# Performance work log

Measured on AMD Instinct MI355X. Metric: run time of the kernel, lower is better.

Reference implementation:

```python
import jax, jax.numpy as jnp
import numpy as np

HEAD_NUM = 16


def setup_inputs() -> dict:
    key = jax.random.key(0)
    ks = jax.random.split(key, 7)
    B, S, D = 4, 2048, 1024
    scale = 1.0 / np.sqrt(D)
    return {
        "q": jax.random.normal(ks[0], (B, S, D), jnp.float32),
        "k": jax.random.normal(ks[1], (B, S, D), jnp.float32),
        "v": jax.random.normal(ks[2], (B, S, D), jnp.float32),
        "w_q": jax.random.normal(ks[3], (D, D), jnp.float32) * scale,
        "w_k": jax.random.normal(ks[4], (D, D), jnp.float32) * scale,
        "w_v": jax.random.normal(ks[5], (D, D), jnp.float32) * scale,
        "w_o": jax.random.normal(ks[6], (D, D), jnp.float32) * scale,
    }


def reference(q, k, v, w_q, w_k, w_v, w_o):
    B, Sq, _ = q.shape
    H = HEAD_NUM
    d_k = w_q.shape[1] // H  # per-head key dim

    def split_heads(x):
        b, s, _ = x.shape
        return x.reshape(b, s, H, -1).transpose(0, 2, 1, 3)  # [b,h,s,d]

    hq = split_heads(q @ w_q)
    hk = split_heads(k @ w_k)
    hv = split_heads(v @ w_v)

    scores = jnp.einsum("bhqd,bhkd->bhqk", hq, hk) / jnp.sqrt(
        jnp.asarray(d_k, dtype=hq.dtype)
    )
    attn = jax.nn.softmax(scores, axis=-1)
    out = jnp.einsum("bhqk,bhkd->bhqd", attn, hv)  # [b,h,q,d]
    out = out.transpose(0, 2, 1, 3).reshape(B, Sq, -1)  # concat heads
    return out @ w_o
```

## Files before the change

### kernel.cpp

```cpp
#include <hip/hip_runtime.h>

typedef unsigned short u16;
typedef short vshort8 __attribute__((ext_vector_type(8)));
typedef __bf16 vbf16x8 __attribute__((ext_vector_type(8)));
typedef float vf32x4 __attribute__((ext_vector_type(4)));
typedef float vf32x16 __attribute__((ext_vector_type(16)));

__device__ __forceinline__ u16 f2bf(float f) {
  unsigned u = __builtin_bit_cast(unsigned, f);
  u += 0x7FFFu + ((u >> 16) & 1u);
  return (u16)(u >> 16);
}

__device__ __forceinline__ unsigned cvtpk(float lo, float hi) {
  unsigned r;
  asm("v_cvt_pk_bf16_f32 %0, %1, %2" : "=v"(r) : "v"(lo), "v"(hi));
  return r;
}

__device__ __forceinline__ vf32x4 mfma_bf16(vshort8 a, vshort8 b, vf32x4 c) {
  return __builtin_amdgcn_mfma_f32_16x16x32_bf16(
      __builtin_bit_cast(vbf16x8, a), __builtin_bit_cast(vbf16x8, b), c, 0, 0, 0);
}

__device__ __forceinline__ vf32x16 mfma32(vshort8 a, vshort8 b, vf32x16 c) {
  return __builtin_amdgcn_mfma_f32_32x32x16_bf16(
      __builtin_bit_cast(vbf16x8, a), __builtin_bit_cast(vbf16x8, b), c, 0, 0, 0);
}

__device__ __forceinline__ void gload16(const void* g, void* l) {
  __builtin_amdgcn_global_load_lds(
      (const __attribute__((address_space(1))) void*)g,
      (__attribute__((address_space(3))) void*)l, 16, 0, 0);
}

__global__ __launch_bounds__(256) void cvtk(const float* __restrict__ in,
                                            u16* __restrict__ out, int n4) {
  int idx = blockIdx.x * 256 + threadIdx.x;
  int stride = gridDim.x * 256;
  for (int i = idx; i < n4; i += stride) {
    float4 v = ((const float4*)in)[i];
    unsigned lo = (unsigned)f2bf(v.x) | ((unsigned)f2bf(v.y) << 16);
    unsigned hi = (unsigned)f2bf(v.z) | ((unsigned)f2bf(v.w) << 16);
    uint2 o; o.x = lo; o.y = hi;
    *(uint2*)&out[(size_t)i * 4] = o;
  }
}

__global__ __launch_bounds__(256) void wtrans(const float* __restrict__ W,
                                              u16* __restrict__ Wt) {
  __shared__ u16 tile[64][72];
  int t = threadIdx.x;
  int n0 = blockIdx.x * 64, k0 = blockIdx.y * 64;
#pragma unroll
  for (int it = 0; it < 4; ++it) {
    int cid = it * 256 + t;
    int r = cid >> 4, c4 = cid & 15;
    float4 v = *(const float4*)&W[(k0 + r) * 1024 + n0 + c4 * 4];
    u16* d = &tile[r][c4 * 4];
    d[0] = f2bf(v.x); d[1] = f2bf(v.y); d[2] = f2bf(v.z); d[3] = f2bf(v.w);
  }
  __syncthreads();
#pragma unroll
  for (int it = 0; it < 4; ++it) {
    int cid = it * 256 + t;
    int rn = cid >> 4, c4 = cid & 15;
    unsigned lo = (unsigned)tile[c4 * 4 + 0][rn] | ((unsigned)tile[c4 * 4 + 1][rn] << 16);
    unsigned hi = (unsigned)tile[c4 * 4 + 2][rn] | ((unsigned)tile[c4 * 4 + 3][rn] << 16);
    uint2 o; o.x = lo; o.y = hi;
    *(uint2*)&Wt[(n0 + rn) * 1024 + k0 + c4 * 4] = o;
  }
}

__global__ __launch_bounds__(256) void vtrans(const u16* __restrict__ V,
                                              u16* __restrict__ Vt) {
  __shared__ u16 tile[64][72];
  int t = threadIdx.x;
  int s0 = blockIdx.x * 64;
  int bh = blockIdx.y, b = bh >> 4, h = bh & 15;
#pragma unroll
  for (int it = 0; it < 2; ++it) {
    int cid = it * 256 + t;
    int r = cid >> 3, c8 = cid & 7;
    vshort8 v = *(const vshort8*)&V[(size_t)(b * 2048 + s0 + r) * 1024 + h * 64 + c8 * 8];
    *(vshort8*)&tile[r][c8 * 8] = v;
  }
  __syncthreads();
#pragma unroll
  for (int it = 0; it < 2; ++it) {
    int cid = it * 256 + t;
    int rd = cid >> 3, c8 = cid & 7;
    unsigned w[4];
#pragma unroll
    for (int j = 0; j < 4; ++j) {
      unsigned lo = tile[c8 * 8 + 2 * j][rd];
      unsigned hi = tile[c8 * 8 + 2 * j + 1][rd];
      w[j] = lo | (hi << 16);
    }
    uint4 o; o.x = w[0]; o.y = w[1]; o.z = w[2]; o.w = w[3];
    *(uint4*)&Vt[(size_t)(bh * 64 + rd) * 2048 + s0 + c8 * 8] = o;
  }
}

template <int OUTF32>
__global__ __launch_bounds__(256) void gemm_nt(const u16* __restrict__ A,
                                               const u16* __restrict__ Bt,
                                               float* __restrict__ Cf,
                                               u16* __restrict__ Cb,
                                               int M, int N, int K, float oscale) {
  __shared__ __align__(16) u16 As[128 * 64];
  __shared__ __align__(16) u16 Bs[128 * 64];
  int t = threadIdx.x, lane = t & 63, wid = t >> 6;
  int g = lane >> 4, i16 = lane & 15;
  int n0 = blockIdx.x * 128, m0 = blockIdx.y * 128;
  int wm = wid >> 1, wn = wid & 1;

  vf32x4 acc[4][4];
#pragma unroll
  for (int a = 0; a < 4; ++a)
#pragma unroll
    for (int b = 0; b < 4; ++b) acc[a][b] = (vf32x4){0.f, 0.f, 0.f, 0.f};

  int ldsbase = (wid * 64) * 8;
  for (int kt = 0; kt < K / 64; ++kt) {
    if (kt) __syncthreads();
#pragma unroll
    for (int it = 0; it < 4; ++it) {
      int cid = it * 256 + t;
      int row = cid >> 3, c = cid & 7, sc = c ^ (row & 7);
      gload16(A + (size_t)(m0 + row) * K + kt * 64 + sc * 8, &As[it * 2048 + ldsbase]);
    }
#pragma unroll
    for (int it = 0; it < 4; ++it) {
      int cid = it * 256 + t;
      int row = cid >> 3, c = cid & 7, sc = c ^ (row & 7);
      gload16(Bt + (size_t)(n0 + row) * K + kt * 64 + sc * 8, &Bs[it * 2048 + ldsbase]);
    }
    __syncthreads();
#pragma unroll
    for (int kc = 0; kc < 2; ++kc) {
      vshort8 af[4], bf[4];
#pragma unroll
      for (int mf = 0; mf < 4; ++mf) {
        int row = wm * 64 + mf * 16 + i16;
        int ch = (kc * 4 + g) ^ (row & 7);
        af[mf] = *(const vshort8*)&As[row * 64 + ch * 8];
      }
#pragma unroll
      for (int nf = 0; nf < 4; ++nf) {
        int row = wn * 64 + nf * 16 + i16;
        int ch = (kc * 4 + g) ^ (row & 7);
        bf[nf] = *(const vshort8*)&Bs[row * 64 + ch * 8];
      }
#pragma unroll
      for (int mf = 0; mf < 4; ++mf)
#pragma unroll
        for (int nf = 0; nf < 4; ++nf)
          acc[mf][nf] = mfma_bf16(af[mf], bf[nf], acc[mf][nf]);
    }
  }
#pragma unroll
  for (int mf = 0; mf < 4; ++mf)
#pragma unroll
    for (int nf = 0; nf < 4; ++nf)
#pragma unroll
      for (int r = 0; r < 4; ++r) {
        int m = m0 + wm * 64 + mf * 16 + g * 4 + r;
        int n = n0 + wn * 64 + nf * 16 + i16;
        if (OUTF32)
          Cf[(size_t)m * N + n] = acc[mf][nf][r] * oscale;
        else
          Cb[(size_t)m * N + n] = f2bf(acc[mf][nf][r] * oscale);
      }
}

__global__ __launch_bounds__(512, 2) void attn_fwd2(const u16* __restrict__ Q,
                                                    const u16* __restrict__ K,
                                                    const u16* __restrict__ Vt,
                                                    u16* __restrict__ O) {
  int t = threadIdx.x, lane = t & 63, w = t >> 6;
  int l31 = lane & 31, hi = lane >> 5;
  int i = blockIdx.x;
  int qb = (i >> 3) & 3;
  int bh = (i & 7) + 8 * (i >> 5);
  int b = bh >> 4, h = bh & 15;

  const u16* Qbase = Q + (size_t)(b * 2048 + qb * 512 + w * 64) * 1024 + h * 64;
  const u16* Kbase = K + (size_t)(b * 2048) * 1024 + h * 64;
  const u16* Vbase = Vt + (size_t)(bh * 64) * 2048;

  vshort8 qf[2][4];
#pragma unroll
  for (int fq = 0; fq < 2; ++fq)
#pragma unroll
    for (int dc = 0; dc < 4; ++dc)
      qf[fq][dc] = *(const vshort8*)&Qbase[(size_t)(fq * 32 + l31) * 1024 + dc * 16 + hi * 8];

  vf32x16 oacc[2][2];
#pragma unroll
  for (int dm = 0; dm < 2; ++dm)
#pragma unroll
    for (int fq = 0; fq < 2; ++fq)
#pragma unroll
      for (int r = 0; r < 16; ++r) oacc[dm][fq][r] = 0.f;
  float mrun[2] = {-3.0e38f, -3.0e38f}, lrun[2] = {0.f, 0.f};

  for (int kt = 0; kt < 32; ++kt) {
    __syncthreads();
    vshort8 kf[2][4], vtf[2][4];
#pragma unroll
    for (int ks = 0; ks < 2; ++ks)
#pragma unroll
      for (int dc = 0; dc < 4; ++dc)
        kf[ks][dc] = *(const vshort8*)&Kbase[(size_t)(kt * 64 + ks * 32 + l31) * 1024 + dc * 16 + hi * 8];
#pragma unroll
    for (int dm = 0; dm < 2; ++dm)
#pragma unroll
      for (int s = 0; s < 4; ++s)
        vtf[dm][s] = *(const vshort8*)&Vbase[(size_t)(dm * 32 + l31) * 2048 + kt * 64 + s * 16 + hi * 8];

    vf32x16 sacc[2][2];
#pragma unroll
    for (int ks = 0; ks < 2; ++ks)
#pragma unroll
      for (int fq = 0; fq < 2; ++fq)
#pragma unroll
        for (int r = 0; r < 16; ++r) sacc[ks][fq][r] = 0.f;

    __builtin_amdgcn_s_setprio(1);
#pragma unroll
    for (int dc = 0; dc < 4; ++dc)
#pragma unroll
      for (int ks = 0; ks < 2; ++ks)
#pragma unroll
        for (int fq = 0; fq < 2; ++fq)
          sacc[ks][fq] = mfma32(kf[ks][dc], qf[fq][dc], sacc[ks][fq]);
    __builtin_amdgcn_s_setprio(0);

#pragma unroll
    for (int fq = 0; fq < 2; ++fq) {
      float pmax = sacc[0][fq][0];
#pragma unroll
      for (int ks = 0; ks < 2; ++ks)
#pragma unroll
        for (int r = 0; r < 16; ++r) pmax = fmaxf(pmax, sacc[ks][fq][r]);
      pmax = fmaxf(pmax, __shfl_xor(pmax, 32));
      float mold = mrun[fq];
      if (pmax > mold + 8.f) {
        float al = exp2f(mold - pmax);
        lrun[fq] *= al;
#pragma unroll
        for (int dm = 0; dm < 2; ++dm)
#pragma unroll
          for (int r = 0; r < 16; ++r) oacc[dm][fq][r] *= al;
        mrun[fq] = pmax;
      }
      float mm = mrun[fq];
      float ssum = 0.f;
#pragma unroll
      for (int ks = 0; ks < 2; ++ks)
#pragma unroll
        for (int r = 0; r < 16; ++r) {
          float p = exp2f(sacc[ks][fq][r] - mm);
          sacc[ks][fq][r] = p;
          ssum += p;
        }
      ssum += __shfl_xor(ssum, 32);
      lrun[fq] += ssum;
    }

#pragma unroll
    for (int s = 0; s < 4; ++s) {
      vshort8 pb[2];
#pragma unroll
      for (int fq = 0; fq < 2; ++fq) {
        const int ks = s >> 1, s1 = s & 1;
        float a0 = sacc[ks][fq][8 * s1 + 0], a1 = sacc[ks][fq][8 * s1 + 1];
        float a2 = sacc[ks][fq][8 * s1 + 2], a3 = sacc[ks][fq][8 * s1 + 3];
        float b0 = sacc[ks][fq][8 * s1 + 4], b1 = sacc[ks][fq][8 * s1 + 5];
        float b2 = sacc[ks][fq][8 * s1 + 6], b3 = sacc[ks][fq][8 * s1 + 7];
        unsigned wA0 = cvtpk(a0, a1), wA1 = cvtpk(a2, a3);
        unsigned wB0 = cvtpk(b0, b1), wB1 = cvtpk(b2, b3);
        unsigned sA0 = hi ? wB0 : wA0, sA1 = hi ? wB1 : wA1;
        unsigned sd0 = hi ? wA0 : wB0, sd1 = hi ? wA1 : wB1;
        unsigned rv0 = __shfl_xor((int)sd0, 32), rv1 = __shfl_xor((int)sd1, 32);
        uint4 wv;
        wv.x = hi ? rv0 : sA0; wv.y = hi ? rv1 : sA1;
        wv.z = hi ? sA0 : rv0; wv.w = hi ? sA1 : rv1;
        pb[fq] = __builtin_bit_cast(vshort8, wv);
      }
      __builtin_amdgcn_s_setprio(1);
#pragma unroll
      for (int dm = 0; dm < 2; ++dm)
#pragma unroll
        for (int fq = 0; fq < 2; ++fq)
          oacc[dm][fq] = mfma32(vtf[dm][s], pb[fq], oacc[dm][fq]);
      __builtin_amdgcn_s_setprio(0);
    }
  }

#pragma unroll
  for (int fq = 0; fq < 2; ++fq) {
    float inv = 1.f / lrun[fq];
    size_t qrow = (size_t)(b * 2048 + qb * 512 + w * 64 + fq * 32 + l31);
#pragma unroll
    for (int dm = 0; dm < 2; ++dm)
#pragma unroll
      for (int u = 0; u < 4; ++u) {
        unsigned w0 = cvtpk(oacc[dm][fq][4 * u + 0] * inv, oacc[dm][fq][4 * u + 1] * inv);
        unsigned w1 = cvtpk(oacc[dm][fq][4 * u + 2] * inv, oacc[dm][fq][4 * u + 3] * inv);
        uint2 o; o.x = w0; o.y = w1;
        *(uint2*)&O[qrow * 1024 + h * 64 + dm * 32 + 8 * u + 4 * hi] = o;
      }
  }
}

extern "C" void kernel_launch(void* const* d_in, const int* in_sizes, int n_in,
                              void* d_out, int out_size, void* d_ws, size_t ws_size,
                              hipStream_t stream) {
  const float* q  = (const float*)d_in[0];
  const float* k  = (const float*)d_in[1];
  const float* v  = (const float*)d_in[2];
  const float* wq = (const float*)d_in[3];
  const float* wk = (const float*)d_in[4];
  const float* wv = (const float*)d_in[5];
  const float* wo = (const float*)d_in[6];
  float* out = (float*)d_out;

  const int M = 8192, D = 1024;
  u16* Qb = (u16*)d_out;
  u16* Kb = Qb + (size_t)M * D;
  u16* xb  = (u16*)d_ws;
  u16* Vb  = xb + (size_t)M * D;
  u16* Vtg = Vb + (size_t)M * D;
  u16* wqt = Vtg + (size_t)M * D;
  u16* wkt = wqt + (size_t)D * D;
  u16* wvt = wkt + (size_t)D * D;
  u16* wot = wvt + (size_t)D * D;

  dim3 blk(256);
  dim3 gw(16, 16);
  wtrans<<<gw, blk, 0, stream>>>(wq, wqt);
  wtrans<<<gw, blk, 0, stream>>>(wk, wkt);
  wtrans<<<gw, blk, 0, stream>>>(wv, wvt);
  wtrans<<<gw, blk, 0, stream>>>(wo, wot);

  const float QSCALE = 0.125f * 1.44269504088896f;
  int n4 = M * D / 4;
  dim3 ggemm(8, 64);
  cvtk<<<2048, blk, 0, stream>>>(q, xb, n4);
  gemm_nt<0><<<ggemm, blk, 0, stream>>>(xb, wqt, nullptr, Qb, M, D, D, QSCALE);
  cvtk<<<2048, blk, 0, stream>>>(k, xb, n4);
  gemm_nt<0><<<ggemm, blk, 0, stream>>>(xb, wkt, nullptr, Kb, M, D, D, 1.0f);
  cvtk<<<2048, blk, 0, stream>>>(v, xb, n4);
  gemm_nt<0><<<ggemm, blk, 0, stream>>>(xb, wvt, nullptr, Vb, M, D, D, 1.0f);

  vtrans<<<dim3(32, 64), blk, 0, stream>>>(Vb, Vtg);
  attn_fwd2<<<dim3(256), dim3(512), 0, stream>>>(Qb, Kb, Vtg, xb );
  gemm_nt<1><<<ggemm, blk, 0, stream>>>(xb, wot, out, nullptr, M, D, D, 1.0f);
}
```

Measured before the change: 311.2 us.

## Split attention into smaller blocks and batch conversion and weight-transpose launches

The attention kernel is restructured so each wave handles one 32-row query fragment instead of two, with 256-thread blocks and a 1024-block grid in place of 256 blocks of 512 threads. This raises the number of blocks and lowers per-wave register use, at the cost of loading K/V fragments twice as often per query row. The four weight-transpose launches are merged into one launch using a z-dimension. The q and k fp32-to-bf16 conversions now run in a single launch, with converted k staged in the Vt buffer before it is needed, which cuts launch count.

Result: slower. 373.6 us (+20.1%).

```diff
diff --git a/kernel.cpp b/kernel.cpp
--- a/kernel.cpp
+++ b/kernel.cpp
@@ -34,8 +34,13 @@
       (__attribute__((address_space(3))) void*)l, 16, 0, 0);
 }
 
-__global__ __launch_bounds__(256) void cvtk(const float* __restrict__ in,
-                                            u16* __restrict__ out, int n4) {
+__global__ __launch_bounds__(256) void cvtk2(const float* __restrict__ a,
+                                             const float* __restrict__ b,
+                                             u16* __restrict__ oa,
+                                             u16* __restrict__ ob, int n4) {
+  const float* in = blockIdx.y ? b : a;
+  u16* out = blockIdx.y ? ob : oa;
+  if (in == nullptr) return;
   int idx = blockIdx.x * 256 + threadIdx.x;
   int stride = gridDim.x * 256;
   for (int i = idx; i < n4; i += stride) {
@@ -47,8 +52,15 @@
   }
 }
 
-__global__ __launch_bounds__(256) void wtrans(const float* __restrict__ W,
-                                              u16* __restrict__ Wt) {
+__global__ __launch_bounds__(256) void wtrans4(const float* __restrict__ w0,
+                                               const float* __restrict__ w1,
+                                               const float* __restrict__ w2,
+                                               const float* __restrict__ w3,
+                                               u16* __restrict__ o0, u16* __restrict__ o1,
+                                               u16* __restrict__ o2, u16* __restrict__ o3) {
+  int z = blockIdx.z;
+  const float* W = z == 0 ? w0 : z == 1 ? w1 : z == 2 ? w2 : w3;
+  u16* Wt = z == 0 ? o0 : z == 1 ? o1 : z == 2 ? o2 : o3;
   __shared__ u16 tile[64][72];
   int t = threadIdx.x;
   int n0 = blockIdx.x * 64, k0 = blockIdx.y * 64;
@@ -174,145 +186,133 @@
       }
 }
 
-__global__ __launch_bounds__(512, 2) void attn_fwd2(const u16* __restrict__ Q,
+__global__ __launch_bounds__(256, 4) void attn_fwd3(const u16* __restrict__ Q,
                                                     const u16* __restrict__ K,
                                                     const u16* __restrict__ Vt,
                                                     u16* __restrict__ O) {
   int t = threadIdx.x, lane = t & 63, w = t >> 6;
   int l31 = lane & 31, hi = lane >> 5;
   int i = blockIdx.x;
-  int qb = (i >> 3) & 3;
-  int bh = (i & 7) + 8 * (i >> 5);
+  int bh = (i & 7) + 8 * (i >> 7);
+  int qc = (i >> 3) & 15;
   int b = bh >> 4, h = bh & 15;
 
-  const u16* Qbase = Q + (size_t)(b * 2048 + qb * 512 + w * 64) * 1024 + h * 64;
+  const u16* Qbase = Q + (size_t)(b * 2048 + qc * 128 + w * 32) * 1024 + h * 64;
   const u16* Kbase = K + (size_t)(b * 2048) * 1024 + h * 64;
   const u16* Vbase = Vt + (size_t)(bh * 64) * 2048;
 
-  vshort8 qf[2][4];
-#pragma unroll
-  for (int fq = 0; fq < 2; ++fq)
-#pragma unroll
-    for (int dc = 0; dc < 4; ++dc)
-      qf[fq][dc] = *(const vshort8*)&Qbase[(size_t)(fq * 32 + l31) * 1024 + dc * 16 + hi * 8];
-
-  vf32x16 oacc[2][2];
+  vshort8 qf[4];
+#pragma unroll
+  for (int dc = 0; dc < 4; ++dc)
+    qf[dc] = *(const vshort8*)&Qbase[(size_t)l31 * 1024 + dc * 16 + hi * 8];
+
+  vf32x16 oacc[2];
 #pragma unroll
   for (int dm = 0; dm < 2; ++dm)
 #pragma unroll
-    for (int fq = 0; fq < 2; ++fq)
-#pragma unroll
-      for (int r = 0; r < 16; ++r) oacc[dm][fq][r] = 0.f;
-  float mrun[2] = {-3.0e38f, -3.0e38f}, lrun[2] = {0.f, 0.f};
+    for (int r = 0; r < 16; ++r) oacc[dm][r] = 0.f;
+  float mrun = -3.0e38f, lrun = 0.f;
 
   for (int kt = 0; kt < 32; ++kt) {
     __syncthreads();
-    vshort8 kf[2][4], vtf[2][4];
+    vshort8 kf[2][4];
 #pragma unroll
     for (int ks = 0; ks < 2; ++ks)
 #pragma unroll
       for (int dc = 0; dc < 4; ++dc)
         kf[ks][dc] = *(const vshort8*)&Kbase[(size_t)(kt * 64 + ks * 32 + l31) * 1024 + dc * 16 + hi * 8];
+
+    vf32x16 sacc[2];
+#pragma unroll
+    for (int ks = 0; ks < 2; ++ks)
+#pragma unroll
+      for (int r = 0; r < 16; ++r) sacc[ks][r] = 0.f;
+
+    __builtin_amdgcn_s_setprio(1);
+#pragma unroll
+    for (int dc = 0; dc < 4; ++dc)
+#pragma unroll
+      for (int ks = 0; ks < 2; ++ks)
+        sacc[ks] = mfma32(kf[ks][dc], qf[dc], sacc[ks]);
+    __builtin_amdgcn_s_setprio(0);
+
+    float tm[8];
+#pragma unroll
+    for (int r = 0; r < 8; ++r)
+      tm[r] = fmaxf(fmaxf(sacc[0][r], sacc[0][r + 8]), fmaxf(sacc[1][r], sacc[1][r + 8]));
+#pragma unroll
+    for (int r = 0; r < 4; ++r) tm[r] = fmaxf(tm[r], tm[r + 4]);
+    float pmax = fmaxf(fmaxf(tm[0], tm[1]), fmaxf(tm[2], tm[3]));
+    pmax = fmaxf(pmax, __shfl_xor(pmax, 32));
+
+    if (pmax > mrun + 8.f) {
+      float al = exp2f(mrun - pmax);
+      lrun *= al;
+#pragma unroll
+      for (int dm = 0; dm < 2; ++dm)
+#pragma unroll
+        for (int r = 0; r < 16; ++r) oacc[dm][r] *= al;
+      mrun = pmax;
+    }
+    float mm = mrun;
+
+    unsigned pk[2][8];
+    float s0 = 0.f, s1 = 0.f, s2 = 0.f, s3 = 0.f;
+#pragma unroll
+    for (int ks = 0; ks < 2; ++ks)
+#pragma unroll
+      for (int u = 0; u < 8; ++u) {
+        float p0 = exp2f(sacc[ks][2 * u] - mm);
+        float p1 = exp2f(sacc[ks][2 * u + 1] - mm);
+        pk[ks][u] = cvtpk(p0, p1);
+        if (u & 1) { s0 += p0; s1 += p1; } else { s2 += p0; s3 += p1; }
+      }
+    float ssum = (s0 + s1) + (s2 + s3);
+    ssum += __shfl_xor(ssum, 32);
+    lrun += ssum;
+
+    vshort8 vtf[2][4];
 #pragma unroll
     for (int dm = 0; dm < 2; ++dm)
 #pragma unroll
       for (int s = 0; s < 4; ++s)
         vtf[dm][s] = *(const vshort8*)&Vbase[(size_t)(dm * 32 + l31) * 2048 + kt * 64 + s * 16 + hi * 8];
 
-    vf32x16 sacc[2][2];
-#pragma unroll
-    for (int ks = 0; ks < 2; ++ks)
-#pragma unroll
-      for (int fq = 0; fq < 2; ++fq)
-#pragma unroll
-        for (int r = 0; r < 16; ++r) sacc[ks][fq][r] = 0.f;
+    vshort8 pb[4];
+#pragma unroll
+    for (int s = 0; s < 4; ++s) {
+      const int ks = s >> 1, s1b = s & 1;
+      unsigned wA0 = pk[ks][4 * s1b + 0], wA1 = pk[ks][4 * s1b + 1];
+      unsigned wB0 = pk[ks][4 * s1b + 2], wB1 = pk[ks][4 * s1b + 3];
+      unsigned sA0 = hi ? wB0 : wA0, sA1 = hi ? wB1 : wA1;
+      unsigned sd0 = hi ? wA0 : wB0, sd1 = hi ? wA1 : wB1;
+      unsigned rv0 = __shfl_xor((int)sd0, 32), rv1 = __shfl_xor((int)sd1, 32);
+      uint4 wv;
+      wv.x = hi ? rv0 : sA0; wv.y = hi ? rv1 : sA1;
+      wv.z = hi ? sA0 : rv0; wv.w = hi ? sA1 : rv1;
+      pb[s] = __builtin_bit_cast(vshort8, wv);
+    }
 
     __builtin_amdgcn_s_setprio(1);
 #pragma unroll
-    for (int dc = 0; dc < 4; ++dc)
-#pragma unroll
-      for (int ks = 0; ks < 2; ++ks)
-#pragma unroll
-        for (int fq = 0; fq < 2; ++fq)
-          sacc[ks][fq] = mfma32(kf[ks][dc], qf[fq][dc], sacc[ks][fq]);
+    for (int s = 0; s < 4; ++s)
+#pragma unroll
+      for (int dm = 0; dm < 2; ++dm)
+        oacc[dm] = mfma32(vtf[dm][s], pb[s], oacc[dm]);
     __builtin_amdgcn_s_setprio(0);
-
-#pragma unroll
-    for (int fq = 0; fq < 2; ++fq) {
-      float pmax = sacc[0][fq][0];
-#pragma unroll
-      for (int ks = 0; ks < 2; ++ks)
-#pragma unroll
-        for (int r = 0; r < 16; ++r) pmax = fmaxf(pmax, sacc[ks][fq][r]);
-      pmax = fmaxf(pmax, __shfl_xor(pmax, 32));
-      float mold = mrun[fq];
-      if (pmax > mold + 8.f) {
-        float al = exp2f(mold - pmax);
-        lrun[fq] *= al;
-#pragma unroll
-        for (int dm = 0; dm < 2; ++dm)
-#pragma unroll
-          for (int r = 0; r < 16; ++r) oacc[dm][fq][r] *= al;
-        mrun[fq] = pmax;
-      }
-      float mm = mrun[fq];
-      float ssum = 0.f;
-#pragma unroll
-      for (int ks = 0; ks < 2; ++ks)
-#pragma unroll
-        for (int r = 0; r < 16; ++r) {
-          float p = exp2f(sacc[ks][fq][r] - mm);
-          sacc[ks][fq][r] = p;
-          ssum += p;
-        }
-      ssum += __shfl_xor(ssum, 32);
-      lrun[fq] += ssum;
-    }
-
-#pragma unroll
-    for (int s = 0; s < 4; ++s) {
-      vshort8 pb[2];
-#pragma unroll
-      for (int fq = 0; fq < 2; ++fq) {
-        const int ks = s >> 1, s1 = s & 1;
-        float a0 = sacc[ks][fq][8 * s1 + 0], a1 = sacc[ks][fq][8 * s1 + 1];
-        float a2 = sacc[ks][fq][8 * s1 + 2], a3 = sacc[ks][fq][8 * s1 + 3];
-        float b0 = sacc[ks][fq][8 * s1 + 4], b1 = sacc[ks][fq][8 * s1 + 5];
-        float b2 = sacc[ks][fq][8 * s1 + 6], b3 = sacc[ks][fq][8 * s1 + 7];
-        unsigned wA0 = cvtpk(a0, a1), wA1 = cvtpk(a2, a3);
-        unsigned wB0 = cvtpk(b0, b1), wB1 = cvtpk(b2, b3);
-        unsigned sA0 = hi ? wB0 : wA0, sA1 = hi ? wB1 : wA1;
-        unsigned sd0 = hi ? wA0 : wB0, sd1 = hi ? wA1 : wB1;
-        unsigned rv0 = __shfl_xor((int)sd0, 32), rv1 = __shfl_xor((int)sd1, 32);
-        uint4 wv;
-        wv.x = hi ? rv0 : sA0; wv.y = hi ? rv1 : sA1;
-        wv.z = hi ? sA0 : rv0; wv.w = hi ? sA1 : rv1;
-        pb[fq] = __builtin_bit_cast(vshort8, wv);
-      }
-      __builtin_amdgcn_s_setprio(1);
-#pragma unroll
-      for (int dm = 0; dm < 2; ++dm)
-#pragma unroll
-        for (int fq = 0; fq < 2; ++fq)
-          oacc[dm][fq] = mfma32(vtf[dm][s], pb[fq], oacc[dm][fq]);
-      __builtin_amdgcn_s_setprio(0);
-    }
-  }
-
-#pragma unroll
-  for (int fq = 0; fq < 2; ++fq) {
-    float inv = 1.f / lrun[fq];
-    size_t qrow = (size_t)(b * 2048 + qb * 512 + w * 64 + fq * 32 + l31);
-#pragma unroll
-    for (int dm = 0; dm < 2; ++dm)
-#pragma unroll
-      for (int u = 0; u < 4; ++u) {
-        unsigned w0 = cvtpk(oacc[dm][fq][4 * u + 0] * inv, oacc[dm][fq][4 * u + 1] * inv);
-        unsigned w1 = cvtpk(oacc[dm][fq][4 * u + 2] * inv, oacc[dm][fq][4 * u + 3] * inv);
-        uint2 o; o.x = w0; o.y = w1;
-        *(uint2*)&O[qrow * 1024 + h * 64 + dm * 32 + 8 * u + 4 * hi] = o;
-      }
-  }
+  }
+
+  float inv = 1.f / lrun;
+  size_t qrow = (size_t)(b * 2048 + qc * 128 + w * 32 + l31);
+#pragma unroll
+  for (int dm = 0; dm < 2; ++dm)
+#pragma unroll
+    for (int u = 0; u < 4; ++u) {
+      unsigned w0 = cvtpk(oacc[dm][4 * u + 0] * inv, oacc[dm][4 * u + 1] * inv);
+      unsigned w1 = cvtpk(oacc[dm][4 * u + 2] * inv, oacc[dm][4 * u + 3] * inv);
+      uint2 o; o.x = w0; o.y = w1;
+      *(uint2*)&O[qrow * 1024 + h * 64 + dm * 32 + 8 * u + 4 * hi] = o;
+    }
 }
 
 extern "C" void kernel_launch(void* const* d_in, const int* in_sizes, int n_in,
@@ -339,23 +339,18 @@
   u16* wot = wvt + (size_t)D * D;
 
   dim3 blk(256);
-  dim3 gw(16, 16);
-  wtrans<<<gw, blk, 0, stream>>>(wq, wqt);
-  wtrans<<<gw, blk, 0, stream>>>(wk, wkt);
-  wtrans<<<gw, blk, 0, stream>>>(wv, wvt);
-  wtrans<<<gw, blk, 0, stream>>>(wo, wot);
+  wtrans4<<<dim3(16, 16, 4), blk, 0, stream>>>(wq, wk, wv, wo, wqt, wkt, wvt, wot);
 
   const float QSCALE = 0.125f * 1.44269504088896f;
   int n4 = M * D / 4;
   dim3 ggemm(8, 64);
-  cvtk<<<2048, blk, 0, stream>>>(q, xb, n4);
+  cvtk2<<<dim3(1024, 2), blk, 0, stream>>>(q, k, xb, Vtg, n4);
   gemm_nt<0><<<ggemm, blk, 0, stream>>>(xb, wqt, nullptr, Qb, M, D, D, QSCALE);
-  cvtk<<<2048, blk, 0, stream>>>(k, xb, n4);
-  gemm_nt<0><<<ggemm, blk, 0, stream>>>(xb, wkt, nullptr, Kb, M, D, D, 1.0f);
-  cvtk<<<2048, blk, 0, stream>>>(v, xb, n4);
+  gemm_nt<0><<<ggemm, blk, 0, stream>>>(Vtg, wkt, nullptr, Kb, M, D, D, 1.0f);
+  cvtk2<<<dim3(1024, 1), blk, 0, stream>>>(v, nullptr, xb, nullptr, n4);
   gemm_nt<0><<<ggemm, blk, 0, stream>>>(xb, wvt, nullptr, Vb, M, D, D, 1.0f);
 
   vtrans<<<dim3(32, 64), blk, 0, stream>>>(Vb, Vtg);
-  attn_fwd2<<<dim3(256), dim3(512), 0, stream>>>(Qb, Kb, Vtg, xb );
+  attn_fwd3<<<dim3(1024), blk, 0, stream>>>(Qb, Kb, Vtg, xb );
   gemm_nt<1><<<ggemm, blk, 0, stream>>>(xb, wot, out, nullptr, M, D, D, 1.0f);
 }
```
